# Kernel tuning notes

Measured on AMD Instinct MI355X. Metric: run time of the kernel, lower is better.

## Reference

```python
import jax, jax.numpy as jnp
import numpy as np

N_ATOM, N_QUERY, KNN = 100000, 20000, 32
E = N_QUERY * KNN
HID, EDGE_F, HEADS = 128, 16, 8
D_HEAD = HID // HEADS
LN_EPS = 1e-5


def setup_inputs() -> dict:
    key = jax.random.key(0)
    ks = jax.random.split(key, 16)
    s = 1.0 / np.sqrt(HID)
    src = jax.random.randint(ks[0], (E,), 0, N_ATOM)
    dst = jnp.repeat(jnp.arange(N_QUERY), KNN)  # each query has KNN incoming edges
    return {
        "h_atom": jax.random.normal(ks[1], (N_ATOM, HID), jnp.float32),
        "h_query": jax.random.normal(ks[2], (N_QUERY, HID), jnp.float32),
        "edge_attr": jax.random.uniform(ks[3], (E, EDGE_F), jnp.float32),
        "W_q": jax.random.normal(ks[4], (HID, HID), jnp.float32) * s,
        "W_k": jax.random.normal(ks[5], (HID, HID), jnp.float32) * s,
        "W_v": jax.random.normal(ks[6], (HID, HID), jnp.float32) * s,
        "W_rbf": jax.random.normal(ks[7], (HEADS, EDGE_F), jnp.float32) * (1.0 / np.sqrt(EDGE_F)),
        "W1": jax.random.normal(ks[8], (HID, 2 * HID), jnp.float32) * (1.0 / np.sqrt(2 * HID)),
        "b1": jnp.zeros((HID,), jnp.float32),
        "W2": jax.random.normal(ks[9], (HID, HID), jnp.float32) * s,
        "b2": jnp.zeros((HID,), jnp.float32),
        "ln_gamma": jnp.ones((HID,), jnp.float32),
        "ln_beta": jnp.zeros((HID,), jnp.float32),
        "edge_index": jnp.stack([src, dst]),
        "n_query": N_QUERY,
    }


def reference(h_atom, h_query, edge_attr, W_q, W_k, W_v, W_rbf, W1, b1, W2, b2,
              ln_gamma, ln_beta, edge_index, n_query):
    src, dst = edge_index[0], edge_index[1]
    En = src.shape[0]
    # gather + project, per-edge multi-head Q/K/V  [E, H, d]
    Q = (h_query[dst] @ W_q.T).reshape(En, HEADS, D_HEAD)
    K = (h_atom[src] @ W_k.T).reshape(En, HEADS, D_HEAD)
    V = (h_atom[src] @ W_v.T).reshape(En, HEADS, D_HEAD)
    scores = jnp.einsum("ehd,ehd->eh", Q, K) / np.sqrt(D_HEAD) + edge_attr @ W_rbf.T  # [E,H]
    # segment softmax over edges sharing the same dst query, per head
    seg_max = jax.lax.stop_gradient(jax.ops.segment_max(scores, dst, num_segments=n_query))
    ex = jnp.exp(scores - seg_max[dst])
    denom = jax.ops.segment_sum(ex, dst, num_segments=n_query)
    alpha = ex / (denom[dst] + 1e-16)  # [E,H]
    # weighted scatter-add aggregation
    msgs = (alpha[:, :, None] * V).reshape(En, HID)
    agg = jax.ops.segment_sum(msgs, dst, num_segments=n_query)  # [Nq, HID]
    # update MLP + residual + LayerNorm
    z = jnp.concatenate([h_query, agg], axis=-1)
    delta = jax.nn.relu(z @ W1.T + b1) @ W2.T + b2
    y = h_query + delta
    mu = y.mean(-1, keepdims=True)
    var = y.var(-1, keepdims=True)
    return (y - mu) / jnp.sqrt(var + LN_EPS) * ln_gamma + ln_beta
```

## Files before the change

kernel.cpp:

```cpp
#include <hip/hip_runtime.h>
#include <hip/hip_bf16.h>
#include <math.h>

#define N_ATOM   100000
#define N_QUERY  20000
#define KNN      32
#define EDGES    (N_QUERY * KNN)

typedef __attribute__((ext_vector_type(8))) short  short8;
typedef __attribute__((ext_vector_type(4))) float  floatx4;
typedef __attribute__((ext_vector_type(2))) float  fx2;

static __device__ __forceinline__ unsigned short f2bf_bits(float f) {
  union { __hip_bfloat16 h; unsigned short u; } cv;
  cv.h = __float2bfloat16(f);
  return cv.u;
}
static __device__ __forceinline__ float bflo(unsigned int u) { return __uint_as_float(u << 16); }
static __device__ __forceinline__ float bfhi(unsigned int u) { return __uint_as_float(u & 0xffff0000u); }

__global__ void pack_all_kernel(const float* __restrict__ Wq, const float* __restrict__ Wk,
                                const float* __restrict__ Wv, const float* __restrict__ W1,
                                const float* __restrict__ W2,
                                const float* __restrict__ edge_attr, const float* __restrict__ Wrbf,
                                unsigned short* __restrict__ WKVp, unsigned short* __restrict__ WQp,
                                unsigned short* __restrict__ W1p,  unsigned short* __restrict__ W2p,
                                float* __restrict__ ED) {
  int tid = blockIdx.x * blockDim.x + threadIdx.x;
  if (tid < 98304) {
    const float *Wa, *Wb; int nsplit, Kd, Nd; unsigned short* dst; float scale = 1.0f;
    int t = tid;
    if (t < 32768)      { Wa = Wk; Wb = Wv; nsplit = 128; Kd = 128; Nd = 256; dst = WKVp; }
    else if (t < 49152) { t -= 32768; Wa = Wq; Wb = Wq; nsplit = 128; Kd = 128; Nd = 128; dst = WQp; scale = 0.25f; }
    else if (t < 81920) { t -= 49152; Wa = W1; Wb = W1; nsplit = 128; Kd = 256; Nd = 128; dst = W1p; }
    else                { t -= 81920; Wa = W2; Wb = W2; nsplit = 128; Kd = 128; Nd = 128; dst = W2p; }
    int j    = t & 7;
    int lane = (t >> 3) & 63;
    int t2   = t >> 9;
    int NT   = Nd >> 4;
    int ntile = t2 % NT;
    int ktile = t2 / NT;
    int k = ktile * 32 + (lane >> 4) * 8 + j;
    int n = ntile * 16 + (lane & 15);
    float v = (n < nsplit) ? Wa[(size_t)n * Kd + k] : Wb[(size_t)(n - nsplit) * Kd + k];
    dst[t] = f2bf_bits(v * scale);
  } else {
    int e = tid - 98304;
    if (e >= EDGES) return;
    const float4* ea = (const float4*)(edge_attr + (size_t)e * 16);
    float4 x0 = ea[0], x1 = ea[1], x2 = ea[2], x3 = ea[3];
    float4 r0, r1;
#pragma unroll
    for (int h = 0; h < 8; h++) {
      const float4* wp = (const float4*)(Wrbf + h * 16);
      float4 w0 = wp[0], w1 = wp[1], w2 = wp[2], w3 = wp[3];
      float d = w0.x*x0.x + w0.y*x0.y + w0.z*x0.z + w0.w*x0.w
              + w1.x*x1.x + w1.y*x1.y + w1.z*x1.z + w1.w*x1.w
              + w2.x*x2.x + w2.y*x2.y + w2.z*x2.z + w2.w*x2.w
              + w3.x*x3.x + w3.y*x3.y + w3.z*x3.z + w3.w*x3.w;
      if (h < 4) ((float*)&r0)[h] = d; else ((float*)&r1)[h - 4] = d;
    }
    float4* dst = (float4*)(ED + (size_t)e * 8);
    dst[0] = r0; dst[1] = r1;
  }
}

__global__ __launch_bounds__(256, 2) void gemm_kvq(
    const float* __restrict__ h_atom, const float* __restrict__ h_query,
    const unsigned short* __restrict__ WKVp, const unsigned short* __restrict__ WQp,
    unsigned char* __restrict__ Kp8, unsigned char* __restrict__ Vp8,
    unsigned short* __restrict__ Qb) {
  constexpr int KB = (N_ATOM + 63) / 64;
  __shared__ unsigned short Wlds[32768];
  const int tid  = threadIdx.x;
  const int l    = tid & 63;
  const int w    = tid >> 6;
  const int quad = l >> 4;
  const int col0 = l & 15;

  if ((int)blockIdx.x < KB) {
    const int row0 = blockIdx.x * 64 + w * 16;
    const int grow = row0 + col0;
    int arow = grow < N_ATOM ? grow : N_ATOM - 1;

    const float* aptr = h_atom + (size_t)arow * 128 + quad * 8;
    floatx4 a[8];
#pragma unroll
    for (int k0 = 0; k0 < 4; k0++) {
      a[2 * k0]     = *(const floatx4*)(aptr + k0 * 32);
      a[2 * k0 + 1] = *(const floatx4*)(aptr + k0 * 32 + 4);
    }

    {
      const uint4* gsrc = (const uint4*)WKVp;
      uint4* ldst = (uint4*)Wlds;
#pragma unroll
      for (int it = 0; it < 16; it++)
        ldst[it * 256 + tid] = gsrc[it * 256 + tid];
    }

    short8 af[4];
#pragma unroll
    for (int k0 = 0; k0 < 4; k0++) {
      af[k0][0] = (short)f2bf_bits(a[2*k0][0]); af[k0][1] = (short)f2bf_bits(a[2*k0][1]);
      af[k0][2] = (short)f2bf_bits(a[2*k0][2]); af[k0][3] = (short)f2bf_bits(a[2*k0][3]);
      af[k0][4] = (short)f2bf_bits(a[2*k0+1][0]); af[k0][5] = (short)f2bf_bits(a[2*k0+1][1]);
      af[k0][6] = (short)f2bf_bits(a[2*k0+1][2]); af[k0][7] = (short)f2bf_bits(a[2*k0+1][3]);
    }
    __syncthreads();

    floatx4 acc[16];
#pragma unroll
    for (int i = 0; i < 16; i++) acc[i] = (floatx4){0.f, 0.f, 0.f, 0.f};
#pragma unroll
    for (int k0 = 0; k0 < 4; k0++) {
      const unsigned short* bbase = Wlds + k0 * 16 * 512 + l * 8;
#pragma unroll
      for (int nt = 0; nt < 16; nt++) {
        short8 bf = *(const short8*)(bbase + nt * 512);
        acc[nt] = __builtin_amdgcn_mfma_f32_16x16x32_bf16(bf, af[k0], acc[nt], 0, 0, 0);
      }
    }

    if (grow < N_ATOM) {
      unsigned char* kbase = Kp8 + (size_t)grow * 128 + quad * 4;
      unsigned char* vbase = Vp8 + (size_t)grow * 128 + quad * 4;
#pragma unroll
      for (int nt = 0; nt < 16; nt++) {
        int pk = __builtin_amdgcn_cvt_pk_fp8_f32(acc[nt][0], acc[nt][1], 0, false);
        pk     = __builtin_amdgcn_cvt_pk_fp8_f32(acc[nt][2], acc[nt][3], pk, true);
        if (nt < 8) *(int*)(kbase + nt * 16) = pk;
        else        *(int*)(vbase + (nt - 8) * 16) = pk;
      }
    }
  } else {
    const int row0 = ((int)blockIdx.x - KB) * 64 + w * 16;
    const int grow = row0 + col0;
    int arow = grow < N_QUERY ? grow : N_QUERY - 1;

    const float* aptr = h_query + (size_t)arow * 128 + quad * 8;
    floatx4 a[8];
#pragma unroll
    for (int k0 = 0; k0 < 4; k0++) {
      a[2 * k0]     = *(const floatx4*)(aptr + k0 * 32);
      a[2 * k0 + 1] = *(const floatx4*)(aptr + k0 * 32 + 4);
    }
    {
      const uint4* gsrc = (const uint4*)WQp;
      uint4* ldst = (uint4*)Wlds;
#pragma unroll
      for (int it = 0; it < 8; it++)
        ldst[it * 256 + tid] = gsrc[it * 256 + tid];
    }
    short8 af[4];
#pragma unroll
    for (int k0 = 0; k0 < 4; k0++) {
      af[k0][0] = (short)f2bf_bits(a[2*k0][0]); af[k0][1] = (short)f2bf_bits(a[2*k0][1]);
      af[k0][2] = (short)f2bf_bits(a[2*k0][2]); af[k0][3] = (short)f2bf_bits(a[2*k0][3]);
      af[k0][4] = (short)f2bf_bits(a[2*k0+1][0]); af[k0][5] = (short)f2bf_bits(a[2*k0+1][1]);
      af[k0][6] = (short)f2bf_bits(a[2*k0+1][2]); af[k0][7] = (short)f2bf_bits(a[2*k0+1][3]);
    }
    __syncthreads();

    floatx4 acc[8];
#pragma unroll
    for (int i = 0; i < 8; i++) acc[i] = (floatx4){0.f, 0.f, 0.f, 0.f};
#pragma unroll
    for (int k0 = 0; k0 < 4; k0++) {
      const unsigned short* bbase = Wlds + k0 * 8 * 512 + l * 8;
#pragma unroll
      for (int nt = 0; nt < 8; nt++) {
        short8 bf = *(const short8*)(bbase + nt * 512);
        acc[nt] = __builtin_amdgcn_mfma_f32_16x16x32_bf16(bf, af[k0], acc[nt], 0, 0, 0);
      }
    }

    if (grow < N_QUERY) {
#pragma unroll
      for (int nt = 0; nt < 8; nt++) {
        unsigned u0 = (unsigned)f2bf_bits(acc[nt][0]) | ((unsigned)f2bf_bits(acc[nt][1]) << 16);
        unsigned u1 = (unsigned)f2bf_bits(acc[nt][2]) | ((unsigned)f2bf_bits(acc[nt][3]) << 16);
        uint2 uu; uu.x = u0; uu.y = u1;
        *(uint2*)(Qb + (size_t)grow * 128 + nt * 16 + quad * 4) = uu;
      }
    }
  }
}

__global__ __launch_bounds__(256, 4) void attn_kernel(
    const unsigned short* __restrict__ Qb,
    const unsigned char* __restrict__ Kp8,
    const unsigned char* __restrict__ Vp8,
    const float* __restrict__ ED,
    const int* __restrict__ src,
    float* __restrict__ Agg) {
  const int l = threadIdx.x & 63;
  const int w = threadIdx.x >> 6;
  const int q = blockIdx.x * 4 + w;
  const int j = l >> 3;
  const int h = l & 7;
  const int e0 = q * KNN;

  int s0 = src[e0 +  0 + j];
  int s1 = src[e0 +  8 + j];
  int s2 = src[e0 + 16 + j];
  int s3 = src[e0 + 24 + j];

  const float* edp = ED + (size_t)e0 * 8 + l;
  float ed0 = edp[0];
  float ed1 = edp[64];
  float ed2 = edp[128];
  float ed3 = edp[192];

  const uint4* qp = (const uint4*)(Qb + (size_t)q * 128 + h * 16);
  uint4 qA = qp[0], qB = qp[1];

  uint4 kq0 = *(const uint4*)(Kp8 + (size_t)s0 * 128 + h * 16);
  uint4 kq1 = *(const uint4*)(Kp8 + (size_t)s1 * 128 + h * 16);
  uint4 kq2 = *(const uint4*)(Kp8 + (size_t)s2 * 128 + h * 16);
  uint4 kq3 = *(const uint4*)(Kp8 + (size_t)s3 * 128 + h * 16);
  uint4 vq0 = *(const uint4*)(Vp8 + (size_t)s0 * 128 + h * 16);
  uint4 vq1 = *(const uint4*)(Vp8 + (size_t)s1 * 128 + h * 16);
  uint4 vq2 = *(const uint4*)(Vp8 + (size_t)s2 * 128 + h * 16);
  uint4 vq3 = *(const uint4*)(Vp8 + (size_t)s3 * 128 + h * 16);

  float qd[16];
  qd[0]  = bflo(qA.x); qd[1]  = bfhi(qA.x); qd[2]  = bflo(qA.y); qd[3]  = bfhi(qA.y);
  qd[4]  = bflo(qA.z); qd[5]  = bfhi(qA.z); qd[6]  = bflo(qA.w); qd[7]  = bfhi(qA.w);
  qd[8]  = bflo(qB.x); qd[9]  = bfhi(qB.x); qd[10] = bflo(qB.y); qd[11] = bfhi(qB.y);
  qd[12] = bflo(qB.z); qd[13] = bfhi(qB.z); qd[14] = bflo(qB.w); qd[15] = bfhi(qB.w);

  float acc[16];
#pragma unroll
  for (int i = 0; i < 16; i++) acc[i] = 0.f;
  float lsum = 0.f;

  auto dopass = [&](const uint4& kq, const uint4& vq, float ed) {
    float kd = 0.f;
    {
      fx2 f0, f1;
      f0 = __builtin_amdgcn_cvt_pk_f32_fp8((int)kq.x, false);
      f1 = __builtin_amdgcn_cvt_pk_f32_fp8((int)kq.x, true);
      kd += qd[0] * f0[0] + qd[1] * f0[1] + qd[2] * f1[0] + qd[3] * f1[1];
      f0 = __builtin_amdgcn_cvt_pk_f32_fp8((int)kq.y, false);
      f1 = __builtin_amdgcn_cvt_pk_f32_fp8((int)kq.y, true);
      kd += qd[4] * f0[0] + qd[5] * f0[1] + qd[6] * f1[0] + qd[7] * f1[1];
      f0 = __builtin_amdgcn_cvt_pk_f32_fp8((int)kq.z, false);
      f1 = __builtin_amdgcn_cvt_pk_f32_fp8((int)kq.z, true);
      kd += qd[8] * f0[0] + qd[9] * f0[1] + qd[10] * f1[0] + qd[11] * f1[1];
      f0 = __builtin_amdgcn_cvt_pk_f32_fp8((int)kq.w, false);
      f1 = __builtin_amdgcn_cvt_pk_f32_fp8((int)kq.w, true);
      kd += qd[12] * f0[0] + qd[13] * f0[1] + qd[14] * f1[0] + qd[15] * f1[1];
    }
    float pe = __expf(kd + ed);
    lsum += pe;
    {
      fx2 g0, g1;
      g0 = __builtin_amdgcn_cvt_pk_f32_fp8((int)vq.x, false);
      g1 = __builtin_amdgcn_cvt_pk_f32_fp8((int)vq.x, true);
      acc[0] += pe * g0[0]; acc[1] += pe * g0[1]; acc[2] += pe * g1[0]; acc[3] += pe * g1[1];
      g0 = __builtin_amdgcn_cvt_pk_f32_fp8((int)vq.y, false);
      g1 = __builtin_amdgcn_cvt_pk_f32_fp8((int)vq.y, true);
      acc[4] += pe * g0[0]; acc[5] += pe * g0[1]; acc[6] += pe * g1[0]; acc[7] += pe * g1[1];
      g0 = __builtin_amdgcn_cvt_pk_f32_fp8((int)vq.z, false);
      g1 = __builtin_amdgcn_cvt_pk_f32_fp8((int)vq.z, true);
      acc[8] += pe * g0[0]; acc[9] += pe * g0[1]; acc[10] += pe * g1[0]; acc[11] += pe * g1[1];
      g0 = __builtin_amdgcn_cvt_pk_f32_fp8((int)vq.w, false);
      g1 = __builtin_amdgcn_cvt_pk_f32_fp8((int)vq.w, true);
      acc[12] += pe * g0[0]; acc[13] += pe * g0[1]; acc[14] += pe * g1[0]; acc[15] += pe * g1[1];
    }
  };
  dopass(kq0, vq0, ed0);
  dopass(kq1, vq1, ed1);
  dopass(kq2, vq2, ed2);
  dopass(kq3, vq3, ed3);

  lsum += __shfl_xor(lsum, 8, 64);
  lsum += __shfl_xor(lsum, 16, 64);
  lsum += __shfl_xor(lsum, 32, 64);

  float r8[8];
  const bool hiA = (l & 32) != 0;
#pragma unroll
  for (int i = 0; i < 8; i++) {
    float keep = hiA ? acc[i + 8] : acc[i];
    float send = hiA ? acc[i]     : acc[i + 8];
    r8[i] = keep + __shfl_xor(send, 32, 64);
  }
  float r4[4];
  const bool hiB = (l & 16) != 0;
#pragma unroll
  for (int i = 0; i < 4; i++) {
    float keep = hiB ? r8[i + 4] : r8[i];
    float send = hiB ? r8[i]     : r8[i + 4];
    r4[i] = keep + __shfl_xor(send, 16, 64);
  }
  float r2[2];
  const bool hiC = (l & 8) != 0;
#pragma unroll
  for (int i = 0; i < 2; i++) {
    float keep = hiC ? r4[i + 2] : r4[i];
    float send = hiC ? r4[i]     : r4[i + 2];
    r2[i] = keep + __shfl_xor(send, 8, 64);
  }
  float inv = 1.f / (lsum + 1e-16f);
  float2 o; o.x = r2[0] * inv; o.y = r2[1] * inv;
  *(float2*)(Agg + (size_t)q * 128 + h * 16 + 2 * j) = o;
}

__global__ __launch_bounds__(256) void mlp_kernel(
    const float* __restrict__ h_query, const float* __restrict__ Agg,
    const unsigned short* __restrict__ W1p, const unsigned short* __restrict__ W2p,
    const float* __restrict__ b1, const float* __restrict__ b2,
    const float* __restrict__ gamma, const float* __restrict__ beta,
    float* __restrict__ out) {
  constexpr int M = N_QUERY;
  constexpr int STRIDE = 136;
  __shared__ unsigned short hid[64 * STRIDE];

  const int l    = threadIdx.x & 63;
  const int w    = threadIdx.x >> 6;
  const int quad = l >> 4;
  const int col0 = l & 15;
  const int row0 = blockIdx.x * 64 + w * 16;
  int arow = row0 + col0;
  if (arow >= M) arow = M - 1;

  floatx4 acc[8];
#pragma unroll
  for (int i = 0; i < 8; i++) acc[i] = (floatx4){0.f, 0.f, 0.f, 0.f};
#pragma unroll
  for (int k0 = 0; k0 < 256; k0 += 32) {
    const float* sp = (k0 < 128) ? (h_query + (size_t)arow * 128 + k0)
                                 : (Agg + (size_t)arow * 128 + (k0 - 128));
    floatx4 a0 = *(const floatx4*)(sp + quad * 8);
    floatx4 a1 = *(const floatx4*)(sp + quad * 8 + 4);
    short8 af;
    af[0] = (short)f2bf_bits(a0[0]); af[1] = (short)f2bf_bits(a0[1]);
    af[2] = (short)f2bf_bits(a0[2]); af[3] = (short)f2bf_bits(a0[3]);
    af[4] = (short)f2bf_bits(a1[0]); af[5] = (short)f2bf_bits(a1[1]);
    af[6] = (short)f2bf_bits(a1[2]); af[7] = (short)f2bf_bits(a1[3]);
    const unsigned short* bbase = W1p + (size_t)(k0 >> 5) * 8 * 512 + l * 8;
#pragma unroll
    for (int nt = 0; nt < 8; nt++) {
      short8 bf = *(const short8*)(bbase + nt * 512);
      acc[nt] = __builtin_amdgcn_mfma_f32_16x16x32_bf16(bf, af, acc[nt], 0, 0, 0);
    }
  }
  {
    const int rl = w * 16 + col0;
#pragma unroll
    for (int nt = 0; nt < 8; nt++) {
      const int c = nt * 16 + quad * 4;
      float4 bb = *(const float4*)(b1 + c);
      unsigned u0 = (unsigned)f2bf_bits(fmaxf(acc[nt][0] + bb.x, 0.f))
                  | ((unsigned)f2bf_bits(fmaxf(acc[nt][1] + bb.y, 0.f)) << 16);
      unsigned u1 = (unsigned)f2bf_bits(fmaxf(acc[nt][2] + bb.z, 0.f))
                  | ((unsigned)f2bf_bits(fmaxf(acc[nt][3] + bb.w, 0.f)) << 16);
      uint2 uu; uu.x = u0; uu.y = u1;
      *(uint2*)(hid + rl * STRIDE + c) = uu;
    }
  }
  __syncthreads();

  floatx4 acc2[8];
#pragma unroll
  for (int i = 0; i < 8; i++) acc2[i] = (floatx4){0.f, 0.f, 0.f, 0.f};
  const int rloc = w * 16 + col0;
#pragma unroll
  for (int k0 = 0; k0 < 128; k0 += 32) {
    short8 af = *(const short8*)(hid + rloc * STRIDE + k0 + quad * 8);
    const unsigned short* bbase = W2p + (size_t)(k0 >> 5) * 8 * 512 + l * 8;
#pragma unroll
    for (int nt = 0; nt < 8; nt++) {
      short8 bf = *(const short8*)(bbase + nt * 512);
      acc2[nt] = __builtin_amdgcn_mfma_f32_16x16x32_bf16(bf, af, acc2[nt], 0, 0, 0);
    }
  }

  const int rowq = row0 + col0;
  const int rr   = rowq < M ? rowq : M - 1;
  float v[8][4];
  float s1 = 0.f, s2 = 0.f;
#pragma unroll
  for (int nt = 0; nt < 8; nt++) {
    const int c = nt * 16 + quad * 4;
    float4 hq = *(const float4*)(h_query + (size_t)rr * 128 + c);
    float4 bb = *(const float4*)(b2 + c);
    float t0 = acc2[nt][0] + bb.x + hq.x;
    float t1 = acc2[nt][1] + bb.y + hq.y;
    float t2 = acc2[nt][2] + bb.z + hq.z;
    float t3 = acc2[nt][3] + bb.w + hq.w;
    v[nt][0] = t0; v[nt][1] = t1; v[nt][2] = t2; v[nt][3] = t3;
    s1 += t0 + t1 + t2 + t3;
    s2 += t0 * t0 + t1 * t1 + t2 * t2 + t3 * t3;
  }
  s1 += __shfl_xor(s1, 16, 64); s1 += __shfl_xor(s1, 32, 64);
  s2 += __shfl_xor(s2, 16, 64); s2 += __shfl_xor(s2, 32, 64);
  float mean = s1 * (1.0f / 128.0f);
  float var  = s2 * (1.0f / 128.0f) - mean * mean;
  float rstd = rsqrtf(var + 1e-5f);
  if (rowq < M) {
#pragma unroll
    for (int nt = 0; nt < 8; nt++) {
      const int c = nt * 16 + quad * 4;
      float4 gg = *(const float4*)(gamma + c);
      float4 be = *(const float4*)(beta + c);
      float4 o;
      o.x = (v[nt][0] - mean) * rstd * gg.x + be.x;
      o.y = (v[nt][1] - mean) * rstd * gg.y + be.y;
      o.z = (v[nt][2] - mean) * rstd * gg.z + be.z;
      o.w = (v[nt][3] - mean) * rstd * gg.w + be.w;
      *(float4*)(out + (size_t)rowq * 128 + c) = o;
    }
  }
}

extern "C" void kernel_launch(void* const* d_in, const int* in_sizes, int n_in,
                              void* d_out, int out_size, void* d_ws, size_t ws_size,
                              hipStream_t stream) {
  const float* h_atom    = (const float*)d_in[0];
  const float* h_query   = (const float*)d_in[1];
  const float* edge_attr = (const float*)d_in[2];
  const float* W_q  = (const float*)d_in[3];
  const float* W_k  = (const float*)d_in[4];
  const float* W_v  = (const float*)d_in[5];
  const float* Wrbf = (const float*)d_in[6];
  const float* W1   = (const float*)d_in[7];
  const float* b1   = (const float*)d_in[8];
  const float* W2   = (const float*)d_in[9];
  const float* b2   = (const float*)d_in[10];
  const float* ln_g = (const float*)d_in[11];
  const float* ln_b = (const float*)d_in[12];
  const int* edge_index = (const int*)d_in[13];
  float* out = (float*)d_out;

  char* ws = (char*)d_ws;
  unsigned char*  Kp8 = (unsigned char*)(ws);
  unsigned char*  Vp8 = (unsigned char*)(ws + 12800000);
  unsigned short* Qb  = (unsigned short*)(ws + 25600000);
  float* Agg          = (float*)(ws + 30720000);
  unsigned short* WKVp = (unsigned short*)(ws + 40960000);
  unsigned short* WQp  = WKVp + 32768;
  unsigned short* W1p  = WQp  + 16384;
  unsigned short* W2p  = W1p  + 32768;
  float* ED           = (float*)(ws + 41160704);

  pack_all_kernel<<<(98304 + EDGES + 255) / 256, 256, 0, stream>>>(
      W_q, W_k, W_v, W1, W2, edge_attr, Wrbf, WKVp, WQp, W1p, W2p, ED);

  constexpr int KB = (N_ATOM + 63) / 64;
  constexpr int QB = (N_QUERY + 63) / 64;
  gemm_kvq<<<KB + QB, 256, 0, stream>>>(h_atom, h_query, WKVp, WQp, Kp8, Vp8, Qb);

  attn_kernel<<<N_QUERY / 4, 256, 0, stream>>>(Qb, Kp8, Vp8, ED, edge_index, Agg);

  mlp_kernel<<<(N_QUERY + 63) / 64, 256, 0, stream>>>(
      h_query, Agg, W1p, W2p, b1, b2, ln_g, ln_b, out);
}
```

Measured before the change: 212.3 us.

## Stage MLP weights through LDS and prefetch all activation rows upfront

```diff
diff --git a/kernel.cpp b/kernel.cpp
--- a/kernel.cpp
+++ b/kernel.cpp
@@ -308,7 +308,7 @@
   *(float2*)(Agg + (size_t)q * 128 + h * 16 + 2 * j) = o;
 }
 
-__global__ __launch_bounds__(256) void mlp_kernel(
+__global__ __launch_bounds__(256, 1) void mlp_kernel(
     const float* __restrict__ h_query, const float* __restrict__ Agg,
     const unsigned short* __restrict__ W1p, const unsigned short* __restrict__ W2p,
     const float* __restrict__ b1, const float* __restrict__ b2,
@@ -316,37 +316,78 @@
     float* __restrict__ out) {
   constexpr int M = N_QUERY;
   constexpr int STRIDE = 136;
+  __shared__ unsigned short Wlds[16384];
   __shared__ unsigned short hid[64 * STRIDE];
 
-  const int l    = threadIdx.x & 63;
-  const int w    = threadIdx.x >> 6;
+  const int tid  = threadIdx.x;
+  const int l    = tid & 63;
+  const int w    = tid >> 6;
   const int quad = l >> 4;
   const int col0 = l & 15;
   const int row0 = blockIdx.x * 64 + w * 16;
-  int arow = row0 + col0;
-  if (arow >= M) arow = M - 1;
+  const int grow = row0 + col0;
+  const int arow = grow < M ? grow : M - 1;
+
+  const float* hp = h_query + (size_t)arow * 128 + quad * 8;
+  const float* gp = Agg     + (size_t)arow * 128 + quad * 8;
+  floatx4 a[16];
+#pragma unroll
+  for (int k0 = 0; k0 < 4; k0++) {
+    a[2*k0]       = *(const floatx4*)(hp + k0 * 32);
+    a[2*k0+1]     = *(const floatx4*)(hp + k0 * 32 + 4);
+    a[8 + 2*k0]   = *(const floatx4*)(gp + k0 * 32);
+    a[8 + 2*k0+1] = *(const floatx4*)(gp + k0 * 32 + 4);
+  }
+
+  {
+    const uint4* gsrc = (const uint4*)W1p;
+    uint4* ldst = (uint4*)Wlds;
+#pragma unroll
+    for (int it = 0; it < 8; it++) ldst[it * 256 + tid] = gsrc[it * 256 + tid];
+  }
+
+  short8 af[8];
+#pragma unroll
+  for (int t = 0; t < 8; t++) {
+    af[t][0] = (short)f2bf_bits(a[2*t][0]);   af[t][1] = (short)f2bf_bits(a[2*t][1]);
+    af[t][2] = (short)f2bf_bits(a[2*t][2]);   af[t][3] = (short)f2bf_bits(a[2*t][3]);
+    af[t][4] = (short)f2bf_bits(a[2*t+1][0]); af[t][5] = (short)f2bf_bits(a[2*t+1][1]);
+    af[t][6] = (short)f2bf_bits(a[2*t+1][2]); af[t][7] = (short)f2bf_bits(a[2*t+1][3]);
+  }
+  __syncthreads();
 
   floatx4 acc[8];
 #pragma unroll
   for (int i = 0; i < 8; i++) acc[i] = (floatx4){0.f, 0.f, 0.f, 0.f};
 #pragma unroll
-  for (int k0 = 0; k0 < 256; k0 += 32) {
-    const float* sp = (k0 < 128) ? (h_query + (size_t)arow * 128 + k0)
-                                 : (Agg + (size_t)arow * 128 + (k0 - 128));
-    floatx4 a0 = *(const floatx4*)(sp + quad * 8);
-    floatx4 a1 = *(const floatx4*)(sp + quad * 8 + 4);
-    short8 af;
-    af[0] = (short)f2bf_bits(a0[0]); af[1] = (short)f2bf_bits(a0[1]);
-    af[2] = (short)f2bf_bits(a0[2]); af[3] = (short)f2bf_bits(a0[3]);
-    af[4] = (short)f2bf_bits(a1[0]); af[5] = (short)f2bf_bits(a1[1]);
-    af[6] = (short)f2bf_bits(a1[2]); af[7] = (short)f2bf_bits(a1[3]);
-    const unsigned short* bbase = W1p + (size_t)(k0 >> 5) * 8 * 512 + l * 8;
+  for (int kt = 0; kt < 4; kt++) {
+    const unsigned short* bbase = Wlds + kt * 4096 + l * 8;
 #pragma unroll
     for (int nt = 0; nt < 8; nt++) {
       short8 bf = *(const short8*)(bbase + nt * 512);
-      acc[nt] = __builtin_amdgcn_mfma_f32_16x16x32_bf16(bf, af, acc[nt], 0, 0, 0);
-    }
-  }
+      acc[nt] = __builtin_amdgcn_mfma_f32_16x16x32_bf16(bf, af[kt], acc[nt], 0, 0, 0);
+    }
+  }
+  __syncthreads();
+
+  {
+    const uint4* gsrc = (const uint4*)(W1p + 16384);
+    uint4* ldst = (uint4*)Wlds;
+#pragma unroll
+    for (int it = 0; it < 8; it++) ldst[it * 256 + tid] = gsrc[it * 256 + tid];
+  }
+  __syncthreads();
+
+#pragma unroll
+  for (int kt = 0; kt < 4; kt++) {
+    const unsigned short* bbase = Wlds + kt * 4096 + l * 8;
+#pragma unroll
+    for (int nt = 0; nt < 8; nt++) {
+      short8 bf = *(const short8*)(bbase + nt * 512);
+      acc[nt] = __builtin_amdgcn_mfma_f32_16x16x32_bf16(bf, af[4 + kt], acc[nt], 0, 0, 0);
+    }
+  }
+
   {
     const int rl = w * 16 + col0;
 #pragma unroll
@@ -363,23 +404,30 @@
   }
   __syncthreads();
 
+  {
+    const uint4* gsrc = (const uint4*)W2p;
+    uint4* ldst = (uint4*)Wlds;
+#pragma unroll
+    for (int it = 0; it < 8; it++) ldst[it * 256 + tid] = gsrc[it * 256 + tid];
+  }
+  __syncthreads();
+
   floatx4 acc2[8];
 #pragma unroll
   for (int i = 0; i < 8; i++) acc2[i] = (floatx4){0.f, 0.f, 0.f, 0.f};
   const int rloc = w * 16 + col0;
 #pragma unroll
   for (int k0 = 0; k0 < 128; k0 += 32) {
-    short8 af = *(const short8*)(hid + rloc * STRIDE + k0 + quad * 8);
-    const unsigned short* bbase = W2p + (size_t)(k0 >> 5) * 8 * 512 + l * 8;
+    short8 af2 = *(const short8*)(hid + rloc * STRIDE + k0 + quad * 8);
+    const unsigned short* bbase = Wlds + (k0 >> 5) * 4096 + l * 8;
 #pragma unroll
     for (int nt = 0; nt < 8; nt++) {
       short8 bf = *(const short8*)(bbase + nt * 512);
-      acc2[nt] = __builtin_amdgcn_mfma_f32_16x16x32_bf16(bf, af, acc2[nt], 0, 0, 0);
-    }
-  }
-
-  const int rowq = row0 + col0;
-  const int rr   = rowq < M ? rowq : M - 1;
+      acc2[nt] = __builtin_amdgcn_mfma_f32_16x16x32_bf16(bf, af2, acc2[nt], 0, 0, 0);
+    }
+  }
+
+  const int rr = grow < M ? grow : M - 1;
   float v[8][4];
   float s1 = 0.f, s2 = 0.f;
 #pragma unroll
@@ -400,7 +448,7 @@
   float mean = s1 * (1.0f / 128.0f);
   float var  = s2 * (1.0f / 128.0f) - mean * mean;
   float rstd = rsqrtf(var + 1e-5f);
-  if (rowq < M) {
+  if (grow < M) {
 #pragma unroll
     for (int nt = 0; nt < 8; nt++) {
       const int c = nt * 16 + quad * 4;
@@ -411,7 +459,7 @@
       o.y = (v[nt][1] - mean) * rstd * gg.y + be.y;
       o.z = (v[nt][2] - mean) * rstd * gg.z + be.z;
       o.w = (v[nt][3] - mean) * rstd * gg.w + be.w;
-      *(float4*)(out + (size_t)rowq * 128 + c) = o;
+      *(float4*)(out + (size_t)grow * 128 + c) = o;
     }
   }
 }
```

After: 210.3 us. About the same (-1.0%).
